# Kernel tuning notes

Measured on AMD Instinct MI355X. Metric: run time of the kernel, lower is better.

## Reference

```python
import jax, jax.numpy as jnp
import numpy as np

TEMPERATURE = 0.5
EPS = 1e-20


def setup_inputs() -> dict:
    key = jax.random.key(0)
    ks = jax.random.split(key, 7)
    N, T, S = 16, 64, 1024
    SRC, TGT, D = 512, 512, 64
    return {
        "input": jax.random.normal(ks[0], (N, T, TGT), jnp.float32),
        "memory_bank": jax.random.normal(ks[1], (N, S, SRC), jnp.float32),
        "W_q": jax.random.normal(ks[2], (TGT, D), jnp.float32) / np.sqrt(TGT),
        "W_ctx": jax.random.normal(ks[3], (SRC, D), jnp.float32) / np.sqrt(SRC),
        "v": jax.random.normal(ks[4], (D,), jnp.float32) / np.sqrt(D),
        "W_out": jax.random.normal(ks[5], (SRC + TGT, TGT), jnp.float32) / np.sqrt(SRC + TGT),
        "b_out": jax.random.normal(ks[6], (TGT,), jnp.float32) * 0.01,
    }


def reference(input, memory_bank, W_q, W_ctx, v, W_out, b_out):
    # MLP attention score: v^T tanh(W_q q + W_ctx h)
    wq = jnp.einsum("ntd,de->nte", input, W_q)            # [N,T,D]
    uh = jnp.einsum("nsd,de->nse", memory_bank, W_ctx)    # [N,S,D]
    wquh = jnp.tanh(wq[:, :, None, :] + uh[:, None, :, :])  # [N,T,S,D]
    scores = jnp.einsum("ntsd,d->nts", wquh, v)           # [N,T,S]

    log_alpha = jax.nn.log_softmax(scores, axis=-1)
    alpha = jnp.exp(log_alpha)                            # c_align_vectors

    # deterministic context + output
    context_c = jnp.einsum("nts,nsd->ntd", alpha, memory_bank)
    h_c = jnp.tanh(jnp.concatenate([input, context_c], axis=-1) @ W_out + b_out)

    # gumbel-softmax sample (K = n_samples = 1, forced by view_as in original)
    u = jax.random.uniform(jax.random.key(42), log_alpha.shape, jnp.float32)
    g = -jnp.log(-jnp.log(u + EPS) + EPS)                 # gumbel noise
    y_align = jax.nn.softmax((log_alpha + g) / TEMPERATURE, axis=-1)  # [N,T,S]

    context_y = jnp.einsum("nts,nsd->ntd", y_align, memory_bank)
    h_y = jnp.tanh(jnp.concatenate([input, context_y], axis=-1) @ W_out + b_out)

    return jnp.stack([h_c, h_y], axis=0)  # [2,N,T,tgt_dim]
```

## Files before the change

### kernel.cpp

```cpp
#include <hip/hip_runtime.h>
#include <hip/hip_bf16.h>
#include <stdint.h>

#define DEV __device__ __forceinline__

typedef __attribute__((ext_vector_type(8))) short short8;
typedef __attribute__((ext_vector_type(4))) float f32x4;

#define TWO_LOG2E 2.8853900817779268f

DEV unsigned short f2bf(float f) {
  uint32_t u = __float_as_uint(f);
  u += 0x7FFFu + ((u >> 16) & 1u);
  return (unsigned short)(u >> 16);
}

DEV uint2 pk4(float4 f) {
  union { __hip_bfloat162 h; unsigned u; } a, b;
  a.h = __float22bfloat162_rn(make_float2(f.x, f.y));
  b.h = __float22bfloat162_rn(make_float2(f.z, f.w));
  return make_uint2(a.u, b.u);
}

DEV short8 mk8(uint2 lo, uint2 hi) {
  union { short8 s; uint4 u; } t;
  t.u = make_uint4(lo.x, lo.y, hi.x, hi.y);
  return t.s;
}

DEV uint32_t rotl32(uint32_t x, int r) { return (x << r) | (x >> (32 - r)); }

DEV void threefry_0_42(uint32_t x0, uint32_t x1, uint32_t& o0, uint32_t& o1) {
  const uint32_t ks0 = 0u, ks1 = 42u, ks2 = 0x1BD11BDAu ^ 42u;
  x0 += ks0; x1 += ks1;
#define TFR(r) { x0 += x1; x1 = rotl32(x1, (r)); x1 ^= x0; }
  TFR(13) TFR(15) TFR(26) TFR(6)  x0 += ks1; x1 += ks2 + 1u;
  TFR(17) TFR(29) TFR(16) TFR(24) x0 += ks2; x1 += ks0 + 2u;
  TFR(13) TFR(15) TFR(26) TFR(6)  x0 += ks0; x1 += ks1 + 3u;
  TFR(17) TFR(29) TFR(16) TFR(24) x0 += ks1; x1 += ks2 + 4u;
  TFR(13) TFR(15) TFR(26) TFR(6)  x0 += ks2; x1 += ks0 + 5u;
#undef TFR
  o0 = x0; o1 = x1;
}

DEV float wredmax(float v) {
#pragma unroll
  for (int off = 32; off > 0; off >>= 1) v = fmaxf(v, __shfl_xor(v, off));
  return v;
}
DEV float wredsum(float v) {
#pragma unroll
  for (int off = 32; off > 0; off >>= 1) v += __shfl_xor(v, off);
  return v;
}

__global__ __launch_bounds__(256) void prep_kernel(const float* __restrict__ Wctx,
                                                   const float* __restrict__ Wq,
                                                   const float* __restrict__ Wout,
                                                   const float* __restrict__ input,
                                                   unsigned short* __restrict__ WctxT,
                                                   unsigned short* __restrict__ WoutT,
                                                   float* __restrict__ wq2) {
  const int b = blockIdx.x;
  const int tid = threadIdx.x;
  __shared__ float tile[64][65];
  __shared__ unsigned short As[64][32];
  if (b < 136) {
    const float* src; unsigned short* dst; int R, C, br, bc;
    if (b < 128) { src = Wout; dst = WoutT; R = 1024; C = 512; br = (b & 15) * 64; bc = (b >> 4) * 64; }
    else         { src = Wctx; dst = WctxT; R = 512;  C = 64;  br = (b - 128) * 64; bc = 0; }
    const int lr = tid >> 4, lc4 = (tid & 15) * 4;
#pragma unroll
    for (int i = 0; i < 4; ++i) {
      float4 v = *(const float4*)(src + (long)(br + lr + i * 16) * C + bc + lc4);
      tile[lr + i * 16][lc4 + 0] = v.x;
      tile[lr + i * 16][lc4 + 1] = v.y;
      tile[lr + i * 16][lc4 + 2] = v.z;
      tile[lr + i * 16][lc4 + 3] = v.w;
    }
    __syncthreads();
#pragma unroll
    for (int i = 0; i < 4; ++i) {
      int crow = lr + i * 16;
      ushort4 o;
      o.x = f2bf(tile[lc4 + 0][crow]);
      o.y = f2bf(tile[lc4 + 1][crow]);
      o.z = f2bf(tile[lc4 + 2][crow]);
      o.w = f2bf(tile[lc4 + 3][crow]);
      *(ushort4*)(dst + (long)(bc + crow) * R + br + lc4) = o;
    }
    return;
  }
  const int mbase = (b - 136) * 64;
  const int srow = tid >> 2, kc = tid & 3;
  const int scol = ((kc ^ (srow & 3)) * 8);
  const int wave = tid >> 6, lane = tid & 63;
  const int wm = (wave >> 1) * 32, wn = (wave & 1) * 32;
  const int q = lane >> 4, r = lane & 15;
  const int c0 = ((q ^ (r & 3)) * 8);
  const float* ap = input + (long)(mbase + srow) * 512 + kc * 8;
  f32x4 acc[2][2];
#pragma unroll
  for (int i = 0; i < 2; ++i)
#pragma unroll
    for (int j = 0; j < 2; ++j) acc[i][j] = (f32x4){0.f, 0.f, 0.f, 0.f};
  for (int k0 = 0; k0 < 512; k0 += 32) {
    float4 fa0 = *(const float4*)(ap + k0);
    float4 fa1 = *(const float4*)(ap + k0 + 4);
    uint2 p0 = pk4(fa0), p1 = pk4(fa1);
    *(uint4*)&As[srow][scol] = make_uint4(p0.x, p0.y, p1.x, p1.y);
    __syncthreads();
    short8 bfrag[2];
#pragma unroll
    for (int j2 = 0; j2 < 2; ++j2) {
      float bv[8];
#pragma unroll
      for (int j = 0; j < 8; ++j)
        bv[j] = Wq[(long)(k0 + q * 8 + j) * 64 + wn + j2 * 16 + r];
      bfrag[j2] = mk8(pk4(make_float4(bv[0], bv[1], bv[2], bv[3])),
                      pk4(make_float4(bv[4], bv[5], bv[6], bv[7])));
    }
    short8 a0 = *(const short8*)&As[wm + r][c0];
    short8 a1 = *(const short8*)&As[wm + 16 + r][c0];
    acc[0][0] = __builtin_amdgcn_mfma_f32_16x16x32_bf16(a0, bfrag[0], acc[0][0], 0, 0, 0);
    acc[0][1] = __builtin_amdgcn_mfma_f32_16x16x32_bf16(a0, bfrag[1], acc[0][1], 0, 0, 0);
    acc[1][0] = __builtin_amdgcn_mfma_f32_16x16x32_bf16(a1, bfrag[0], acc[1][0], 0, 0, 0);
    acc[1][1] = __builtin_amdgcn_mfma_f32_16x16x32_bf16(a1, bfrag[1], acc[1][1], 0, 0, 0);
    __syncthreads();
  }
#pragma unroll
  for (int i2 = 0; i2 < 2; ++i2)
#pragma unroll
    for (int j2 = 0; j2 < 2; ++j2) {
      int gcol = wn + j2 * 16 + r;
#pragma unroll
      for (int reg = 0; reg < 4; ++reg)
        wq2[(long)(mbase + wm + i2 * 16 + q * 4 + reg) * 64 + gcol] =
            acc[i2][j2][reg] * TWO_LOG2E;
    }
}

__global__ __launch_bounds__(256) void gemm_uh_scores(const float* __restrict__ mb,
                                                      const unsigned short* __restrict__ WctxT,
                                                      const float* __restrict__ wq2,
                                                      const float* __restrict__ v,
                                                      float* __restrict__ sc) {
  __shared__ unsigned short As[64][32];
  __shared__ unsigned short Bs[64][32];
  __shared__ float uhs[64][65];
  __shared__ float wqs[4096];
  __shared__ float vs[64];
  const int tid = threadIdx.x;
  const int m0 = blockIdx.x * 64;
  const int n = m0 >> 10, s0 = m0 & 1023;
  const int srow = tid >> 2, kc = tid & 3;
  const int scol = ((kc ^ (srow & 3)) * 8);
  const int wave = tid >> 6, lane = tid & 63;
  const int wm = (wave >> 1) * 32, wn = (wave & 1) * 32;
  const int q = lane >> 4, r = lane & 15;
  const int c0 = ((q ^ (r & 3)) * 8);
  const float* ap = mb + (long)(m0 + srow) * 512 + kc * 8;
  const unsigned short* bp = WctxT + (long)srow * 512 + kc * 8;

#pragma unroll
  for (int i = 0; i < 4; ++i)
    *(float4*)&wqs[i * 1024 + tid * 4] = *(const float4*)(wq2 + (long)n * 4096 + i * 1024 + tid * 4);
  if (tid < 64) vs[tid] = v[tid];

  f32x4 acc[2][2];
#pragma unroll
  for (int i = 0; i < 2; ++i)
#pragma unroll
    for (int j = 0; j < 2; ++j) acc[i][j] = (f32x4){0.f, 0.f, 0.f, 0.f};

  float4 fa0 = *(const float4*)(ap);
  float4 fa1 = *(const float4*)(ap + 4);
  uint4 fb = *(const uint4*)(bp);
  for (int k0 = 0; k0 < 512; k0 += 32) {
    uint2 p0 = pk4(fa0), p1 = pk4(fa1);
    *(uint4*)&As[srow][scol] = make_uint4(p0.x, p0.y, p1.x, p1.y);
    *(uint4*)&Bs[srow][scol] = fb;
    __syncthreads();
    if (k0 + 32 < 512) {
      fa0 = *(const float4*)(ap + k0 + 32);
      fa1 = *(const float4*)(ap + k0 + 36);
      fb = *(const uint4*)(bp + k0 + 32);
    }
    short8 a0 = *(const short8*)&As[wm + r][c0];
    short8 a1 = *(const short8*)&As[wm + 16 + r][c0];
    short8 b0 = *(const short8*)&Bs[wn + r][c0];
    short8 b1 = *(const short8*)&Bs[wn + 16 + r][c0];
    acc[0][0] = __builtin_amdgcn_mfma_f32_16x16x32_bf16(a0, b0, acc[0][0], 0, 0, 0);
    acc[0][1] = __builtin_amdgcn_mfma_f32_16x16x32_bf16(a0, b1, acc[0][1], 0, 0, 0);
    acc[1][0] = __builtin_amdgcn_mfma_f32_16x16x32_bf16(a1, b0, acc[1][0], 0, 0, 0);
    acc[1][1] = __builtin_amdgcn_mfma_f32_16x16x32_bf16(a1, b1, acc[1][1], 0, 0, 0);
    __syncthreads();
  }
#pragma unroll
  for (int i2 = 0; i2 < 2; ++i2)
#pragma unroll
    for (int j2 = 0; j2 < 2; ++j2)
#pragma unroll
      for (int reg = 0; reg < 4; ++reg)
        uhs[wm + i2 * 16 + q * 4 + reg][wn + j2 * 16 + r] = acc[i2][j2][reg] * TWO_LOG2E;
  __syncthreads();

  const int s = tid & 63;
  const int tbase = (tid >> 6) * 16;
  float sumv = 0.f;
#pragma unroll
  for (int c = 0; c < 64; c += 4) {
    float4 vv = *(const float4*)&vs[c];
    sumv += vv.x + vv.y + vv.z + vv.w;
  }
  float* scp = sc + (long)(n * 64 + tbase) * 1024 + s0 + s;
#pragma unroll
  for (int tg = 0; tg < 16; tg += 4) {
    const float* w0 = &wqs[(tbase + tg + 0) * 64];
    const float* w1 = &wqs[(tbase + tg + 1) * 64];
    const float* w2 = &wqs[(tbase + tg + 2) * 64];
    const float* w3 = &wqs[(tbase + tg + 3) * 64];
    float a0 = 0.f, a1 = 0.f, a2 = 0.f, a3 = 0.f;
    for (int c = 0; c < 64; ++c) {
      float u = uhs[s][c];
      float vvc = vs[c];
      a0 = fmaf(vvc, __builtin_amdgcn_rcpf(1.f + __builtin_amdgcn_exp2f(u + w0[c])), a0);
      a1 = fmaf(vvc, __builtin_amdgcn_rcpf(1.f + __builtin_amdgcn_exp2f(u + w1[c])), a1);
      a2 = fmaf(vvc, __builtin_amdgcn_rcpf(1.f + __builtin_amdgcn_exp2f(u + w2[c])), a2);
      a3 = fmaf(vvc, __builtin_amdgcn_rcpf(1.f + __builtin_amdgcn_exp2f(u + w3[c])), a3);
    }
    scp[(long)(tg + 0) * 1024] = fmaf(-2.f, a0, sumv);
    scp[(long)(tg + 1) * 1024] = fmaf(-2.f, a1, sumv);
    scp[(long)(tg + 2) * 1024] = fmaf(-2.f, a2, sumv);
    scp[(long)(tg + 3) * 1024] = fmaf(-2.f, a3, sumv);
  }
}

__global__ __launch_bounds__(256) void softmax_gumbel(const float* __restrict__ sc,
                                                      float* __restrict__ alpha_g,
                                                      float* __restrict__ y_g) {
  const int tid = threadIdx.x;
  const int nt = blockIdx.x;
  __shared__ float red[4];
  float4 l4 = *(const float4*)(sc + (long)nt * 1024 + tid * 4);
  float lsc[4] = {l4.x, l4.y, l4.z, l4.w};

  const int wv = tid >> 6, ln = tid & 63;
  float m = fmaxf(fmaxf(lsc[0], lsc[1]), fmaxf(lsc[2], lsc[3]));
  m = wredmax(m);
  if (ln == 0) red[wv] = m;
  __syncthreads();
  m = fmaxf(fmaxf(red[0], red[1]), fmaxf(red[2], red[3]));
  __syncthreads();
  float ss = 0.f;
#pragma unroll
  for (int i = 0; i < 4; ++i) ss += __expf(lsc[i] - m);
  ss = wredsum(ss);
  if (ln == 0) red[wv] = ss;
  __syncthreads();
  ss = red[0] + red[1] + red[2] + red[3];
  const float logl = __logf(ss);
  __syncthreads();

  const uint32_t jbase = (uint32_t)nt * 1024u + (uint32_t)tid * 4u;
  float ys[4];
  float4 av;
#pragma unroll
  for (int i = 0; i < 4; ++i) {
    float la = lsc[i] - m - logl;
    ((float*)&av)[i] = __expf(la);
    uint32_t o0, o1;
    threefry_0_42(0u, jbase + i, o0, o1);
    uint32_t bits = o0 ^ o1;
    float u = __uint_as_float((bits >> 9) | 0x3f800000u) - 1.0f;
    float g = -__logf(-__logf(u + 1e-20f) + 1e-20f);
    ys[i] = (la + g) * 2.0f;
  }
  *(float4*)(alpha_g + (long)nt * 1024 + tid * 4) = av;

  float m2 = fmaxf(fmaxf(ys[0], ys[1]), fmaxf(ys[2], ys[3]));
  m2 = wredmax(m2);
  if (ln == 0) red[wv] = m2;
  __syncthreads();
  m2 = fmaxf(fmaxf(red[0], red[1]), fmaxf(red[2], red[3]));
  __syncthreads();
  float s2 = 0.f;
  float4 ye;
#pragma unroll
  for (int i = 0; i < 4; ++i) { ((float*)&ye)[i] = __expf(ys[i] - m2); s2 += ((float*)&ye)[i]; }
  s2 = wredsum(s2);
  if (ln == 0) red[wv] = s2;
  __syncthreads();
  s2 = red[0] + red[1] + red[2] + red[3];
  const float rinv = __fdividef(1.f, s2);
  ye.x *= rinv; ye.y *= rinv; ye.z *= rinv; ye.w *= rinv;
  *(float4*)(y_g + (long)nt * 1024 + tid * 4) = ye;
}

__global__ __launch_bounds__(256) void gemm_ctx_mfma(const float* __restrict__ alpha,
                                                     const float* __restrict__ yal,
                                                     const float* __restrict__ mb,
                                                     float* __restrict__ ctx) {
  __shared__ unsigned short As[64][32];
  const int tid = threadIdx.x;
  const int vt = blockIdx.x >> 4, n = blockIdx.x & 15;
  const int dbase = blockIdx.y * 32;
  const int srow = tid >> 2, kc = tid & 3;
  const int scol = ((kc ^ (srow & 3)) * 8);
  const int wave = tid >> 6, lane = tid & 63;
  const int wm = (wave >> 1) * 32, wn = (wave & 1) * 16;
  const int q = lane >> 4, r = lane & 15;
  const int c0 = ((q ^ (r & 3)) * 8);
  const float* Abase = (vt == 0 ? alpha : yal) + (long)n * 65536;
  const float* ap = Abase + (long)srow * 1024 + kc * 8;
  const float* bcol = mb + (long)n * 524288 + dbase + wn + r;
  f32x4 acc[2];
  acc[0] = (f32x4){0.f, 0.f, 0.f, 0.f};
  acc[1] = (f32x4){0.f, 0.f, 0.f, 0.f};

  float4 fa0 = *(const float4*)(ap);
  float4 fa1 = *(const float4*)(ap + 4);
  float bv[8];
#pragma unroll
  for (int j = 0; j < 8; ++j) bv[j] = bcol[(long)(q * 8 + j) * 512];

  for (int k0 = 0; k0 < 1024; k0 += 32) {
    uint2 p0 = pk4(fa0), p1 = pk4(fa1);
    *(uint4*)&As[srow][scol] = make_uint4(p0.x, p0.y, p1.x, p1.y);
    __syncthreads();
    float4 blo = make_float4(bv[0], bv[1], bv[2], bv[3]);
    float4 bhi = make_float4(bv[4], bv[5], bv[6], bv[7]);
    short8 b0 = mk8(pk4(blo), pk4(bhi));
    if (k0 + 32 < 1024) {
      fa0 = *(const float4*)(ap + k0 + 32);
      fa1 = *(const float4*)(ap + k0 + 36);
#pragma unroll
      for (int j = 0; j < 8; ++j) bv[j] = bcol[(long)(k0 + 32 + q * 8 + j) * 512];
    }
    short8 a0 = *(const short8*)&As[wm + r][c0];
    short8 a1 = *(const short8*)&As[wm + 16 + r][c0];
    acc[0] = __builtin_amdgcn_mfma_f32_16x16x32_bf16(a0, b0, acc[0], 0, 0, 0);
    acc[1] = __builtin_amdgcn_mfma_f32_16x16x32_bf16(a1, b0, acc[1], 0, 0, 0);
    __syncthreads();
  }
#pragma unroll
  for (int i2 = 0; i2 < 2; ++i2) {
    int gcol = dbase + wn + r;
#pragma unroll
    for (int reg = 0; reg < 4; ++reg) {
      long grow = (long)vt * 1024 + n * 64 + wm + i2 * 16 + q * 4 + reg;
      ctx[grow * 512 + gcol] = acc[i2][reg];
    }
  }
}

__global__ __launch_bounds__(256) void gemm_out_mfma(const float* __restrict__ input,
                                                     const float* __restrict__ ctx,
                                                     const unsigned short* __restrict__ WoutT,
                                                     const float* __restrict__ bout,
                                                     float* __restrict__ out) {
  __shared__ unsigned short As[64][32];
  __shared__ unsigned short Bs[32][32];
  const int tid = threadIdx.x;
  const int mbase = blockIdx.x * 64, nbase = blockIdx.y * 32;
  const int srow = tid >> 2, kc = tid & 3;
  const int scol = ((kc ^ (srow & 3)) * 8);
  const int wave = tid >> 6, lane = tid & 63;
  const int wm = (wave >> 1) * 32, wn = (wave & 1) * 16;
  const int q = lane >> 4, r = lane & 15;
  const int c0 = ((q ^ (r & 3)) * 8);
  const int vv = mbase >> 10, nt = (mbase + srow) & 1023;
  const float* ap_lo = input + (long)nt * 512 + kc * 8;
  const float* ap_hi = ctx + (long)(vv * 1024 + nt) * 512 + kc * 8 - 512;
  const int brow = (tid & 127) >> 2;
  const unsigned short* bp = WoutT + (long)(nbase + brow) * 1024 + kc * 8;
  f32x4 acc[2];
  acc[0] = (f32x4){0.f, 0.f, 0.f, 0.f};
  acc[1] = (f32x4){0.f, 0.f, 0.f, 0.f};

  float4 fa0 = *(const float4*)(ap_lo);
  float4 fa1 = *(const float4*)(ap_lo + 4);
  uint4 fb;
  if (tid < 128) fb = *(const uint4*)(bp);
  for (int k0 = 0; k0 < 1024; k0 += 32) {
    uint2 p0 = pk4(fa0), p1 = pk4(fa1);
    *(uint4*)&As[srow][scol] = make_uint4(p0.x, p0.y, p1.x, p1.y);
    if (tid < 128) *(uint4*)&Bs[brow][(kc ^ (brow & 3)) * 8] = fb;
    __syncthreads();
    int kn = k0 + 32;
    if (kn < 1024) {
      const float* apn = (kn < 512) ? ap_lo : ap_hi;
      fa0 = *(const float4*)(apn + kn);
      fa1 = *(const float4*)(apn + kn + 4);
      if (tid < 128) fb = *(const uint4*)(bp + kn);
    }
    short8 a0 = *(const short8*)&As[wm + r][c0];
    short8 a1 = *(const short8*)&As[wm + 16 + r][c0];
    short8 b0 = *(const short8*)&Bs[wn + r][c0];
    acc[0] = __builtin_amdgcn_mfma_f32_16x16x32_bf16(a0, b0, acc[0], 0, 0, 0);
    acc[1] = __builtin_amdgcn_mfma_f32_16x16x32_bf16(a1, b0, acc[1], 0, 0, 0);
    __syncthreads();
  }
#pragma unroll
  for (int i2 = 0; i2 < 2; ++i2) {
    int gcol = nbase + wn + r;
    float bb = bout[gcol];
#pragma unroll
    for (int reg = 0; reg < 4; ++reg) {
      int grow = mbase + wm + i2 * 16 + q * 4 + reg;
      float z = acc[i2][reg] + bb;
      float rc = __builtin_amdgcn_rcpf(1.f + __builtin_amdgcn_exp2f(z * TWO_LOG2E));
      out[(long)grow * 512 + gcol] = fmaf(-2.f, rc, 1.f);
    }
  }
}

extern "C" void kernel_launch(void* const* d_in, const int* in_sizes, int n_in,
                              void* d_out, int out_size, void* d_ws, size_t ws_size,
                              hipStream_t stream) {
  const float* input = (const float*)d_in[0];
  const float* mb    = (const float*)d_in[1];
  const float* W_q   = (const float*)d_in[2];
  const float* W_ctx = (const float*)d_in[3];
  const float* v     = (const float*)d_in[4];
  const float* W_out = (const float*)d_in[5];
  const float* b_out = (const float*)d_in[6];
  float* out = (float*)d_out;
  float* ws = (float*)d_ws;

  float* sc    = ws;
  float* wq2   = ws + 1048576;
  float* yal   = ws + 1114112;
  unsigned short* WctxT = (unsigned short*)(ws + 2162688);
  unsigned short* WoutT = (unsigned short*)(ws + 2179072);
  float* alpha = out;
  float* ctx   = sc;

  prep_kernel<<<152, 256, 0, stream>>>(W_ctx, W_q, W_out, input, WctxT, WoutT, wq2);
  gemm_uh_scores<<<256, 256, 0, stream>>>(mb, WctxT, wq2, v, sc);
  softmax_gumbel<<<1024, 256, 0, stream>>>(sc, alpha, yal);
  gemm_ctx_mfma<<<dim3(32, 16), 256, 0, stream>>>(alpha, yal, mb, ctx);
  gemm_out_mfma<<<dim3(32, 16), 256, 0, stream>>>(input, ctx, WoutT, b_out, out);
}
```

Baseline: 174.3 us.

## Split uh GEMM from score computation and tile scores over more blocks

Splits the fused uh-GEMM plus tanh-score kernel into two kernels. The GEMM writes a transposed uh to global memory. A separate scores kernel with a 3D grid of 1024 blocks computes 4 query rows per thread instead of 16. The aim is to spread the transcendental-heavy score stage over more blocks and waves for better latency hiding and occupancy. The cost is an extra launch and a 4 MB global write/read round trip for uh.

```diff
diff --git a/kernel.cpp b/kernel.cpp
--- a/kernel.cpp
+++ b/kernel.cpp
@@ -140,33 +140,21 @@
     }
 }
 
-__global__ __launch_bounds__(256) void gemm_uh_scores(const float* __restrict__ mb,
-                                                      const unsigned short* __restrict__ WctxT,
-                                                      const float* __restrict__ wq2,
-                                                      const float* __restrict__ v,
-                                                      float* __restrict__ sc) {
+__global__ __launch_bounds__(256) void gemm_uh(const float* __restrict__ mb,
+                                               const unsigned short* __restrict__ WctxT,
+                                               float* __restrict__ uhT) {
   __shared__ unsigned short As[64][32];
   __shared__ unsigned short Bs[64][32];
-  __shared__ float uhs[64][65];
-  __shared__ float wqs[4096];
-  __shared__ float vs[64];
-  const int tid = threadIdx.x;
-  const int m0 = blockIdx.x * 64;
-  const int n = m0 >> 10, s0 = m0 & 1023;
+  const int tid = threadIdx.x;
+  const int mbase = blockIdx.x * 64;
   const int srow = tid >> 2, kc = tid & 3;
   const int scol = ((kc ^ (srow & 3)) * 8);
   const int wave = tid >> 6, lane = tid & 63;
   const int wm = (wave >> 1) * 32, wn = (wave & 1) * 32;
   const int q = lane >> 4, r = lane & 15;
   const int c0 = ((q ^ (r & 3)) * 8);
-  const float* ap = mb + (long)(m0 + srow) * 512 + kc * 8;
+  const float* ap = mb + (long)(mbase + srow) * 512 + kc * 8;
   const unsigned short* bp = WctxT + (long)srow * 512 + kc * 8;
-
-#pragma unroll
-  for (int i = 0; i < 4; ++i)
-    *(float4*)&wqs[i * 1024 + tid * 4] = *(const float4*)(wq2 + (long)n * 4096 + i * 1024 + tid * 4);
-  if (tid < 64) vs[tid] = v[tid];
-
   f32x4 acc[2][2];
 #pragma unroll
   for (int i = 0; i < 2; ++i)
@@ -199,41 +187,69 @@
 #pragma unroll
   for (int i2 = 0; i2 < 2; ++i2)
 #pragma unroll
-    for (int j2 = 0; j2 < 2; ++j2)
-#pragma unroll
-      for (int reg = 0; reg < 4; ++reg)
-        uhs[wm + i2 * 16 + q * 4 + reg][wn + j2 * 16 + r] = acc[i2][j2][reg] * TWO_LOG2E;
-  __syncthreads();
-
-  const int s = tid & 63;
-  const int tbase = (tid >> 6) * 16;
+    for (int j2 = 0; j2 < 2; ++j2) {
+      int gcol = wn + j2 * 16 + r;
+      int m = mbase + wm + i2 * 16 + q * 4;
+      int n = m >> 10, s0 = m & 1023;
+      float4 o;
+      o.x = acc[i2][j2][0] * TWO_LOG2E;
+      o.y = acc[i2][j2][1] * TWO_LOG2E;
+      o.z = acc[i2][j2][2] * TWO_LOG2E;
+      o.w = acc[i2][j2][3] * TWO_LOG2E;
+      *(float4*)(uhT + (long)n * 65536 + (long)gcol * 1024 + s0) = o;
+    }
+}
+
+__global__ __launch_bounds__(256) void scores_tile(const float* __restrict__ uhT,
+                                                   const float* __restrict__ wq2,
+                                                   const float* __restrict__ v,
+                                                   float* __restrict__ sc) {
+  __shared__ float uhs[64][68];
+  __shared__ float wqs[16][64];
+  __shared__ float vs[64];
+  const int tid = threadIdx.x;
+  const int s0 = blockIdx.x * 64, tb = blockIdx.y * 16, n = blockIdx.z;
+
+  *(float4*)(&wqs[0][0] + tid * 4) =
+      *(const float4*)(wq2 + ((long)n * 64 + tb) * 64 + tid * 4);
+  if (tid < 64) vs[tid] = v[tid];
+  {
+    const int dr = tid >> 4, c4 = (tid & 15) * 4;
+#pragma unroll
+    for (int dk = 0; dk < 4; ++dk) {
+      int d = dk * 16 + dr;
+      *(float4*)&uhs[d][c4] = *(const float4*)(uhT + (long)n * 65536 + (long)d * 1024 + s0 + c4);
+    }
+  }
+  __syncthreads();
+
   float sumv = 0.f;
 #pragma unroll
   for (int c = 0; c < 64; c += 4) {
     float4 vv = *(const float4*)&vs[c];
     sumv += vv.x + vv.y + vv.z + vv.w;
   }
-  float* scp = sc + (long)(n * 64 + tbase) * 1024 + s0 + s;
-#pragma unroll
-  for (int tg = 0; tg < 16; tg += 4) {
-    const float* w0 = &wqs[(tbase + tg + 0) * 64];
-    const float* w1 = &wqs[(tbase + tg + 1) * 64];
-    const float* w2 = &wqs[(tbase + tg + 2) * 64];
-    const float* w3 = &wqs[(tbase + tg + 3) * 64];
-    float a0 = 0.f, a1 = 0.f, a2 = 0.f, a3 = 0.f;
-    for (int c = 0; c < 64; ++c) {
-      float u = uhs[s][c];
-      float vvc = vs[c];
-      a0 = fmaf(vvc, __builtin_amdgcn_rcpf(1.f + __builtin_amdgcn_exp2f(u + w0[c])), a0);
-      a1 = fmaf(vvc, __builtin_amdgcn_rcpf(1.f + __builtin_amdgcn_exp2f(u + w1[c])), a1);
-      a2 = fmaf(vvc, __builtin_amdgcn_rcpf(1.f + __builtin_amdgcn_exp2f(u + w2[c])), a2);
-      a3 = fmaf(vvc, __builtin_amdgcn_rcpf(1.f + __builtin_amdgcn_exp2f(u + w3[c])), a3);
-    }
-    scp[(long)(tg + 0) * 1024] = fmaf(-2.f, a0, sumv);
-    scp[(long)(tg + 1) * 1024] = fmaf(-2.f, a1, sumv);
-    scp[(long)(tg + 2) * 1024] = fmaf(-2.f, a2, sumv);
-    scp[(long)(tg + 3) * 1024] = fmaf(-2.f, a3, sumv);
-  }
+
+  const int s = tid & 63, wv = tid >> 6;
+  const float* w0 = &wqs[wv * 4 + 0][0];
+  const float* w1 = &wqs[wv * 4 + 1][0];
+  const float* w2 = &wqs[wv * 4 + 2][0];
+  const float* w3 = &wqs[wv * 4 + 3][0];
+  float a0 = 0.f, a1 = 0.f, a2 = 0.f, a3 = 0.f;
+#pragma unroll 16
+  for (int d = 0; d < 64; ++d) {
+    float u = uhs[d][s];
+    float vd = vs[d];
+    a0 = fmaf(vd, __builtin_amdgcn_rcpf(1.f + __builtin_amdgcn_exp2f(u + w0[d])), a0);
+    a1 = fmaf(vd, __builtin_amdgcn_rcpf(1.f + __builtin_amdgcn_exp2f(u + w1[d])), a1);
+    a2 = fmaf(vd, __builtin_amdgcn_rcpf(1.f + __builtin_amdgcn_exp2f(u + w2[d])), a2);
+    a3 = fmaf(vd, __builtin_amdgcn_rcpf(1.f + __builtin_amdgcn_exp2f(u + w3[d])), a3);
+  }
+  float* scp = sc + ((long)n * 64 + tb + wv * 4) * 1024 + s0 + s;
+  scp[0]    = fmaf(-2.f, a0, sumv);
+  scp[1024] = fmaf(-2.f, a1, sumv);
+  scp[2048] = fmaf(-2.f, a2, sumv);
+  scp[3072] = fmaf(-2.f, a3, sumv);
 }
 
 __global__ __launch_bounds__(256) void softmax_gumbel(const float* __restrict__ sc,
@@ -428,16 +444,18 @@
   float* out = (float*)d_out;
   float* ws = (float*)d_ws;
 
-  float* sc    = ws;
+  float* uhT   = ws;
   float* wq2   = ws + 1048576;
   float* yal   = ws + 1114112;
-  unsigned short* WctxT = (unsigned short*)(ws + 2162688);
-  unsigned short* WoutT = (unsigned short*)(ws + 2179072);
+  float* sc    = ws + 2162688;
+  unsigned short* WctxT = (unsigned short*)(ws + 3211264);
+  unsigned short* WoutT = (unsigned short*)(ws + 3227648);
   float* alpha = out;
-  float* ctx   = sc;
+  float* ctx   = uhT;
 
   prep_kernel<<<152, 256, 0, stream>>>(W_ctx, W_q, W_out, input, WctxT, WoutT, wq2);
-  gemm_uh_scores<<<256, 256, 0, stream>>>(mb, WctxT, wq2, v, sc);
+  gemm_uh<<<256, 256, 0, stream>>>(mb, WctxT, uhT);
+  scores_tile<<<dim3(16, 4, 16), 256, 0, stream>>>(uhT, wq2, v, sc);
   softmax_gumbel<<<1024, 256, 0, stream>>>(sc, alpha, yal);
   gemm_ctx_mfma<<<dim3(32, 16), 256, 0, stream>>>(alpha, yal, mb, ctx);
   gemm_out_mfma<<<dim3(32, 16), 256, 0, stream>>>(input, ctx, WoutT, b_out, out);
```

Result: faster. 165.5 us (-5.1%).
